# Performance work log

Measured on AMD Instinct MI355X. Metric: run time of the kernel, lower is better.

The kernel has to match this reference:

```python
import jax, jax.numpy as jnp
import numpy as np

GORDER = 8
IN_DIM = 32768
CLASSES = 10


def setup_inputs() -> dict:
    key = jax.random.key(0)
    k1, k2 = jax.random.split(key)
    x = jax.random.normal(k1, (2048, IN_DIM), dtype=jnp.float32)
    weight = jax.random.normal(k2, (CLASSES, IN_DIM), dtype=jnp.float32)
    radius = jnp.ones((1,), dtype=jnp.float32)
    return {"x": x, "weight": weight, "radius": radius}


def reference(x, weight, radius):
    # theta = 2*pi/gorder * value
    c = jnp.float32(2.0 * np.pi / GORDER)
    tx = c * x            # (B, K)
    tw = c * weight       # (O, K)
    # GroupSim: radius * sum_i cos(tw[o,i] - tx[b,i])
    #         = radius * (cos(tx) @ cos(tw)^T + sin(tx) @ sin(tw)^T)
    sims = jnp.einsum('bk,ok->bo', jnp.cos(tx), jnp.cos(tw)) \
         + jnp.einsum('bk,ok->bo', jnp.sin(tx), jnp.sin(tw))
    sims = radius[0] * sims
    return sims * jnp.float32(1.0 / IN_DIM ** 0.5)
```

## Files before the change

kernel.cpp:

```cpp
#include <hip/hip_runtime.h>


typedef _Float16 half2_t __attribute__((ext_vector_type(2)));
typedef _Float16 half8_t __attribute__((ext_vector_type(8)));
typedef float f32x4 __attribute__((ext_vector_type(4)));

#define K_DIM 32768
#define B_DIM 2048
#define O_DIM 10
#define NWIN 2048
#define KCH 64
#define WPC (NWIN / KCH)
#define ITERS (WPC / 2)
#define MTILES (B_DIM / 64)
#define THREADS 256
#define INV_SQRT_K 0.005524271728019903f


__device__ __forceinline__ half2_t pack_cs(float c, float s) {
    return __builtin_bit_cast(half2_t, __builtin_amdgcn_cvt_pkrtz(c, s));
}

__device__ __forceinline__ half8_t afrag(float4 xc) {
    const float* xf = (const float*)&xc;
    uint4 au;
    unsigned u[4];
    #pragma unroll
    for (int j = 0; j < 4; ++j) {
        float rr = xf[j] * 0.125f;
        u[j] = __builtin_bit_cast(unsigned,
                   pack_cs(__builtin_amdgcn_cosf(rr),
                           __builtin_amdgcn_sinf(rr)));
    }
    au.x = u[0]; au.y = u[1]; au.z = u[2]; au.w = u[3];
    return __builtin_bit_cast(half8_t, au);
}

__global__ void wtab_kernel(const float* __restrict__ w,
                            uint4* __restrict__ wtab,
                            float* __restrict__ out) {
    if (blockIdx.x < (B_DIM * O_DIM) / THREADS)
        out[blockIdx.x * THREADS + threadIdx.x] = 0.f;

    int gid = blockIdx.x * THREADS + threadIdx.x;
    int t = gid >> 6, l = gid & 63;
    int o = l & 15, kg = l >> 4;
    int k = t * 16 + kg * 4;
    uint4 v; v.x = v.y = v.z = v.w = 0u;
    if (o < O_DIM) {
        const float4 wv = *(const float4*)(w + (size_t)o * K_DIM + k);
        const float* wp = (const float*)&wv;
        unsigned u[4];
        #pragma unroll
        for (int j = 0; j < 4; ++j) {
            float rr = wp[j] * 0.125f;
            u[j] = __builtin_bit_cast(unsigned,
                       pack_cs(__builtin_amdgcn_cosf(rr),
                               __builtin_amdgcn_sinf(rr)));
        }
        v.x = u[0]; v.y = u[1]; v.z = u[2]; v.w = u[3];
    }
    wtab[gid] = v;
}

__global__ __launch_bounds__(THREADS) void gsim_mfma(
        const float* __restrict__ x,
        const uint4* __restrict__ wtab,
        const float* __restrict__ radius,
        float* __restrict__ out) {
    const int bid = blockIdx.x;
    const int mt = bid & (MTILES - 1);
    const int kc = bid >> 5;
    const int t = threadIdx.x;
    const int wave = t >> 6, lane = t & 63;
    const int o = lane & 15, kg = lane >> 4;

    const int row = mt * 64 + wave * 16 + o;
    const int t0 = kc * WPC;
    const float4* xp = (const float4*)x + ((size_t)row * (K_DIM / 4) + t0 * 4 + kg);
    const uint4* bp = wtab + (size_t)t0 * 64 + lane;

    f32x4 acc = {0.f, 0.f, 0.f, 0.f};

    float4 xc0 = xp[0], xc1 = xp[4];
    uint4  bc0 = bp[0], bc1 = bp[64];

    #pragma unroll 1
    for (int i = 0; i < ITERS; ++i) {
        const int ni = (i + 1 < ITERS) ? (i + 1) : i;
        float4 xn0 = xp[ni * 8],       xn1 = xp[ni * 8 + 4];
        uint4  bn0 = bp[ni * 128],     bn1 = bp[ni * 128 + 64];

        half8_t a0 = afrag(xc0);
        acc = __builtin_amdgcn_mfma_f32_16x16x32_f16(
                  a0, __builtin_bit_cast(half8_t, bc0), acc, 0, 0, 0);
        half8_t a1 = afrag(xc1);
        acc = __builtin_amdgcn_mfma_f32_16x16x32_f16(
                  a1, __builtin_bit_cast(half8_t, bc1), acc, 0, 0, 0);

        xc0 = xn0; xc1 = xn1; bc0 = bn0; bc1 = bn1;
    }

    if (o < O_DIM) {
        const float sc = radius[0] * INV_SQRT_K;
        const int rbase = mt * 64 + wave * 16 + kg * 4;
        #pragma unroll
        for (int reg = 0; reg < 4; ++reg)
            atomicAdd(out + (size_t)(rbase + reg) * O_DIM + o, acc[reg] * sc);
    }
}

extern "C" void kernel_launch(void* const* d_in, const int* in_sizes, int n_in,
                              void* d_out, int out_size, void* d_ws, size_t ws_size,
                              hipStream_t stream) {
    const float* x      = (const float*)d_in[0];
    const float* w      = (const float*)d_in[1];
    const float* radius = (const float*)d_in[2];
    float* out = (float*)d_out;

    uint4* wtab = (uint4*)d_ws;

    hipLaunchKernelGGL(wtab_kernel, dim3(NWIN * 64 / THREADS), dim3(THREADS),
                       0, stream, w, wtab, out);
    hipLaunchKernelGGL(gsim_mfma, dim3(MTILES * KCH), dim3(THREADS),
                       0, stream, x, wtab, radius, out);
}
```

Before: 55.88 us.

## Stage x tiles through LDS with async global_load_lds double buffering

Swaps direct per-lane float4 register loads of x for asynchronous global-to-LDS loads (global_load_lds) into a double-buffered shared tile. The tile uses an XOR swizzle to avoid bank conflicts. Each step prefetches the next 64-column chunk while 4 MFMAs consume the current one, and the weight-table loads are batched per step. The aim is to get coalesced row-contiguous global reads and overlap memory latency with compute. The cost is extra __syncthreads and LDS traffic per step.

```diff
diff --git a/kernel.cpp b/kernel.cpp
--- a/kernel.cpp
+++ b/kernel.cpp
@@ -11,7 +11,9 @@
 #define NWIN 2048
 #define KCH 64
 #define WPC (NWIN / KCH)
-#define ITERS (WPC / 2)
+#define BK 64
+#define STEPS 8
+#define WINS 4
 #define MTILES (B_DIM / 64)
 #define THREADS 256
 #define INV_SQRT_K 0.005524271728019903f
@@ -34,6 +36,13 @@
     }
     au.x = u[0]; au.y = u[1]; au.z = u[2]; au.w = u[3];
     return __builtin_bit_cast(half8_t, au);
+}
+
+__device__ __forceinline__ void gl_lds16(const float* g, float* l) {
+    __builtin_amdgcn_global_load_lds(
+        (const __attribute__((address_space(1))) unsigned int*)g,
+        (__attribute__((address_space(3))) unsigned int*)l,
+        16, 0, 0);
 }
 
 __global__ void wtab_kernel(const float* __restrict__ w,
@@ -68,6 +77,8 @@
         const uint4* __restrict__ wtab,
         const float* __restrict__ radius,
         float* __restrict__ out) {
+    __shared__ float xtile[2][64 * BK];
+
     const int bid = blockIdx.x;
     const int mt = bid & (MTILES - 1);
     const int kc = bid >> 5;
@@ -75,30 +86,51 @@
     const int wave = t >> 6, lane = t & 63;
     const int o = lane & 15, kg = lane >> 4;
 
-    const int row = mt * 64 + wave * 16 + o;
-    const int t0 = kc * WPC;
-    const float4* xp = (const float4*)x + ((size_t)row * (K_DIM / 4) + t0 * 4 + kg);
-    const uint4* bp = wtab + (size_t)t0 * 64 + lane;
+    const int srh = lane >> 4;
+    const int su  = lane & 15;
+    const float* gx = x + (size_t)(mt * 64 + wave * 16 + srh) * K_DIM + kc * 512;
+
+    const int o7 = o & 7;
+
+    const uint4* bp = wtab + (size_t)(kc * WPC) * 64 + lane;
 
     f32x4 acc = {0.f, 0.f, 0.f, 0.f};
 
-    float4 xc0 = xp[0], xc1 = xp[4];
-    uint4  bc0 = bp[0], bc1 = bp[64];
+    #pragma unroll
+    for (int i = 0; i < 4; ++i) {
+        const int r7 = (i * 4 + srh) & 7;
+        gl_lds16(gx + (size_t)(i * 4) * K_DIM + ((su ^ r7) << 2),
+                 &xtile[0][wave * 1024 + i * 256]);
+    }
 
-    #pragma unroll 1
-    for (int i = 0; i < ITERS; ++i) {
-        const int ni = (i + 1 < ITERS) ? (i + 1) : i;
-        float4 xn0 = xp[ni * 8],       xn1 = xp[ni * 8 + 4];
-        uint4  bn0 = bp[ni * 128],     bn1 = bp[ni * 128 + 64];
+    #pragma unroll
+    for (int s = 0; s < STEPS; ++s) {
+        __syncthreads();
 
-        half8_t a0 = afrag(xc0);
-        acc = __builtin_amdgcn_mfma_f32_16x16x32_f16(
-                  a0, __builtin_bit_cast(half8_t, bc0), acc, 0, 0, 0);
-        half8_t a1 = afrag(xc1);
-        acc = __builtin_amdgcn_mfma_f32_16x16x32_f16(
-                  a1, __builtin_bit_cast(half8_t, bc1), acc, 0, 0, 0);
+        if (s + 1 < STEPS) {
+            #pragma unroll
+            for (int i = 0; i < 4; ++i) {
+                const int r7 = (i * 4 + srh) & 7;
+                gl_lds16(gx + (size_t)(i * 4) * K_DIM + (s + 1) * BK
+                            + ((su ^ r7) << 2),
+                         &xtile[(s + 1) & 1][wave * 1024 + i * 256]);
+            }
+        }
 
-        xc0 = xn0; xc1 = xn1; bc0 = bn0; bc1 = bn1;
+        uint4 bc[WINS];
+        #pragma unroll
+        for (int j = 0; j < WINS; ++j)
+            bc[j] = bp[(size_t)(s * WINS + j) * 64];
+
+        #pragma unroll
+        for (int win = 0; win < WINS; ++win) {
+            const float4 xv = *(const float4*)
+                &xtile[s & 1][wave * 1024 + o * 64
+                              + ((((win << 2) + kg) ^ o7) << 2)];
+            acc = __builtin_amdgcn_mfma_f32_16x16x32_f16(
+                      afrag(xv), __builtin_bit_cast(half8_t, bc[win]),
+                      acc, 0, 0, 0);
+        }
     }
 
     if (o < O_DIM) {
```

New measurement: 55.77 us. Within noise of the previous version (-0.2%).
